# Optimization experiments

Measured on AMD Instinct MI355X. Metric: run time of the kernel, lower is better.

## Reference

```python
import jax, jax.numpy as jnp
import numpy as np

N = 1_000_000
D1 = 16          # n_input_1 (first-layer features, cols 0:16)
D2 = 16          # n_input_2 (second-layer features, cols 16:32)
NC = 64          # n_clusters (first layer)
NCPC = 8         # n_clusters_per_cluster (second layer)


def setup_inputs() -> dict:
    key = jax.random.key(0)
    k1, k2, k3 = jax.random.split(key, 3)
    x = jax.random.normal(k1, (N, D1 + D2), dtype=jnp.float32)
    centers_outer = jax.random.normal(k2, (NC, D1), dtype=jnp.float32)
    centers_inner = jax.random.normal(k3, (NC, NCPC, D2), dtype=jnp.float32)
    return {"x": x, "centers_outer": centers_outer, "centers_inner": centers_inner}


def reference(x, centers_outer, centers_inner):
    # x: [N, D1+D2]; input_1_idx = cols [0:D1], input_2_idx = cols [D1:D1+D2]
    x1 = x[:, :D1]
    x2 = x[:, D1:]

    # First-layer nearest-centroid assignment (squared Euclidean).
    # ||x1 - c||^2 = ||x1||^2 - 2 x1.c + ||c||^2; the ||x1||^2 term is
    # constant over clusters so it does not affect the argmin.
    d1 = jnp.sum(centers_outer ** 2, axis=-1)[None, :] - 2.0 * (x1 @ centers_outer.T)  # [N, NC]
    outer = jnp.argmin(d1, axis=1)  # [N] int

    # Second-layer assignment: each sample only compares against the NCPC
    # sub-centers of its outer cluster (this fuses the original per-cluster
    # torch.where gather/scatter loop into one vectorized pass).
    sub = centers_inner[outer]  # [N, NCPC, D2] gather
    d2 = jnp.sum(sub ** 2, axis=-1) - 2.0 * jnp.einsum("nd,nkd->nk", x2, sub)  # [N, NCPC]
    inner = jnp.argmin(d2, axis=1)  # [N]

    return inner + outer * NCPC  # combined cluster id in [0, NC*NCPC)
```

## Files before the change

kernel.cpp:

```cpp
#include <hip/hip_runtime.h>

constexpr int D = 16;
constexpr int NC = 64;
constexpr int NCPC = 8;
constexpr int OSTRIDE = NCPC * D + 4;
constexpr int NPT = 4;
constexpr int BLOCK = 256;

__global__ __launch_bounds__(BLOCK, 4)
void cluster_kernel(const float* __restrict__ x,
                    const float* __restrict__ co,
                    const float* __restrict__ ci,
                    int* __restrict__ out, int n)
{
    __shared__ __align__(16) float s_ci[NC * OSTRIDE];
    __shared__ __align__(16) float s_onorm[NC];
    __shared__ float s_inorm[NC * 9];

    const int t = threadIdx.x;

    const float4* ci4 = (const float4*)ci;
    #pragma unroll
    for (int i = 0; i < 8; ++i) {
        int idx = t + i * BLOCK;
        int o = idx >> 5;
        int f = idx & 31;
        float4 v = ci4[idx];
        *(float4*)&s_ci[o * OSTRIDE + f * 4] = v;
    }
    for (int i = t; i < NC + NC * NCPC; i += BLOCK) {
        const float* src = (i < NC) ? (co + i * D) : (ci + (i - NC) * D);
        float s = 0.f;
        #pragma unroll
        for (int k = 0; k < D; ++k) s = fmaf(src[k], src[k], s);
        if (i < NC) {
            s_onorm[i] = s;
        } else {
            int ii = i - NC;
            s_inorm[(ii >> 3) * 9 + (ii & 7)] = s;
        }
    }
    __syncthreads();

    const int base = blockIdx.x * (BLOCK * NPT) + t;
    #pragma unroll 1
    for (int it = 0; it < NPT; ++it) {
        int p = base + it * BLOCK;
        if (p < n) {
            const float4* xp = (const float4*)(x + (size_t)p * 32);
            float4 xa = xp[0], xb = xp[1], xc = xp[2], xd = xp[3];
            float4 ya = xp[4], yb = xp[5], yc = xp[6], yd = xp[7];
            float x1[16] = {xa.x,xa.y,xa.z,xa.w, xb.x,xb.y,xb.z,xb.w,
                            xc.x,xc.y,xc.z,xc.w, xd.x,xd.y,xd.z,xd.w};
            float x2[16] = {ya.x,ya.y,ya.z,ya.w, yb.x,yb.y,yb.z,yb.w,
                            yc.x,yc.y,yc.z,yc.w, yd.x,yd.y,yd.z,yd.w};

            float bestd = 3.4e38f;
            int bo = 0;
            #pragma unroll
            for (int jt = 0; jt < NC / 4; ++jt) {
                float4 nn = *(const float4*)&s_onorm[jt * 4];
                #pragma unroll
                for (int jj = 0; jj < 4; ++jj) {
                    int j = jt * 4 + jj;
                    const float* c = co + j * D;
                    float dot = 0.f;
                    #pragma unroll
                    for (int k = 0; k < D; ++k) dot = fmaf(x1[k], c[k], dot);
                    float nrm = (jj == 0) ? nn.x : (jj == 1) ? nn.y : (jj == 2) ? nn.z : nn.w;
                    float d = fmaf(-2.f, dot, nrm);
                    if (d < bestd) { bestd = d; bo = j; }
                }
            }

            const float* cb = s_ci + bo * OSTRIDE;
            const float* nb = s_inorm + bo * 9;
            float bestd2 = 3.4e38f;
            int bk = 0;
            #pragma unroll
            for (int k = 0; k < NCPC; ++k) {
                float4 c0 = *(const float4*)&cb[k * D + 0];
                float4 c1 = *(const float4*)&cb[k * D + 4];
                float4 c2 = *(const float4*)&cb[k * D + 8];
                float4 c3 = *(const float4*)&cb[k * D + 12];
                float dot = 0.f;
                dot = fmaf(x2[0],  c0.x, dot); dot = fmaf(x2[1],  c0.y, dot);
                dot = fmaf(x2[2],  c0.z, dot); dot = fmaf(x2[3],  c0.w, dot);
                dot = fmaf(x2[4],  c1.x, dot); dot = fmaf(x2[5],  c1.y, dot);
                dot = fmaf(x2[6],  c1.z, dot); dot = fmaf(x2[7],  c1.w, dot);
                dot = fmaf(x2[8],  c2.x, dot); dot = fmaf(x2[9],  c2.y, dot);
                dot = fmaf(x2[10], c2.z, dot); dot = fmaf(x2[11], c2.w, dot);
                dot = fmaf(x2[12], c3.x, dot); dot = fmaf(x2[13], c3.y, dot);
                dot = fmaf(x2[14], c3.z, dot); dot = fmaf(x2[15], c3.w, dot);
                float d = fmaf(-2.f, dot, nb[k]);
                if (d < bestd2) { bestd2 = d; bk = k; }
            }

            out[p] = bo * NCPC + bk;
        }
    }
}

extern "C" void kernel_launch(void* const* d_in, const int* in_sizes, int n_in,
                              void* d_out, int out_size, void* d_ws, size_t ws_size,
                              hipStream_t stream) {
    const float* x  = (const float*)d_in[0];
    const float* co = (const float*)d_in[1];
    const float* ci = (const float*)d_in[2];
    int* out = (int*)d_out;
    int n = in_sizes[0] / 32;
    int blocks = (n + BLOCK * NPT - 1) / (BLOCK * NPT);
    cluster_kernel<<<blocks, BLOCK, 0, stream>>>(x, co, ci, out, n);
}
```

Measured before the change: 199.0 us.

## Process four points per thread jointly to reuse outer centroid loads

```diff
diff --git a/kernel.cpp b/kernel.cpp
--- a/kernel.cpp
+++ b/kernel.cpp
@@ -20,84 +20,93 @@
     const int t = threadIdx.x;
 
     const float4* ci4 = (const float4*)ci;
-    #pragma unroll
+#pragma unroll
     for (int i = 0; i < 8; ++i) {
         int idx = t + i * BLOCK;
         int o = idx >> 5;
         int f = idx & 31;
-        float4 v = ci4[idx];
-        *(float4*)&s_ci[o * OSTRIDE + f * 4] = v;
+        *(float4*)&s_ci[o * OSTRIDE + f * 4] = ci4[idx];
     }
     for (int i = t; i < NC + NC * NCPC; i += BLOCK) {
-        const float* src = (i < NC) ? (co + i * D) : (ci + (i - NC) * D);
+        const float* src = (i < NC) ? (co + i * D) : (ci + (size_t)(i - NC) * D);
         float s = 0.f;
-        #pragma unroll
+#pragma unroll
         for (int k = 0; k < D; ++k) s = fmaf(src[k], src[k], s);
-        if (i < NC) {
-            s_onorm[i] = s;
-        } else {
-            int ii = i - NC;
-            s_inorm[(ii >> 3) * 9 + (ii & 7)] = s;
-        }
+        if (i < NC) s_onorm[i] = s;
+        else { int ii = i - NC; s_inorm[(ii >> 3) * 9 + (ii & 7)] = s; }
     }
     __syncthreads();
 
     const int base = blockIdx.x * (BLOCK * NPT) + t;
-    #pragma unroll 1
-    for (int it = 0; it < NPT; ++it) {
-        int p = base + it * BLOCK;
-        if (p < n) {
-            const float4* xp = (const float4*)(x + (size_t)p * 32);
-            float4 xa = xp[0], xb = xp[1], xc = xp[2], xd = xp[3];
-            float4 ya = xp[4], yb = xp[5], yc = xp[6], yd = xp[7];
-            float x1[16] = {xa.x,xa.y,xa.z,xa.w, xb.x,xb.y,xb.z,xb.w,
-                            xc.x,xc.y,xc.z,xc.w, xd.x,xd.y,xd.z,xd.w};
-            float x2[16] = {ya.x,ya.y,ya.z,ya.w, yb.x,yb.y,yb.z,yb.w,
-                            yc.x,yc.y,yc.z,yc.w, yd.x,yd.y,yd.z,yd.w};
 
-            float bestd = 3.4e38f;
-            int bo = 0;
-            #pragma unroll
-            for (int jt = 0; jt < NC / 4; ++jt) {
-                float4 nn = *(const float4*)&s_onorm[jt * 4];
-                #pragma unroll
-                for (int jj = 0; jj < 4; ++jj) {
-                    int j = jt * 4 + jj;
-                    const float* c = co + j * D;
-                    float dot = 0.f;
-                    #pragma unroll
-                    for (int k = 0; k < D; ++k) dot = fmaf(x1[k], c[k], dot);
-                    float nrm = (jj == 0) ? nn.x : (jj == 1) ? nn.y : (jj == 2) ? nn.z : nn.w;
-                    float d = fmaf(-2.f, dot, nrm);
-                    if (d < bestd) { bestd = d; bo = j; }
-                }
-            }
+    int p[NPT];
+    bool valid[NPT];
+#pragma unroll
+    for (int pt = 0; pt < NPT; ++pt) {
+        int pp = base + pt * BLOCK;
+        valid[pt] = pp < n;
+        p[pt] = valid[pt] ? pp : (n - 1);
+    }
 
-            const float* cb = s_ci + bo * OSTRIDE;
-            const float* nb = s_inorm + bo * 9;
-            float bestd2 = 3.4e38f;
-            int bk = 0;
-            #pragma unroll
-            for (int k = 0; k < NCPC; ++k) {
-                float4 c0 = *(const float4*)&cb[k * D + 0];
-                float4 c1 = *(const float4*)&cb[k * D + 4];
-                float4 c2 = *(const float4*)&cb[k * D + 8];
-                float4 c3 = *(const float4*)&cb[k * D + 12];
-                float dot = 0.f;
-                dot = fmaf(x2[0],  c0.x, dot); dot = fmaf(x2[1],  c0.y, dot);
-                dot = fmaf(x2[2],  c0.z, dot); dot = fmaf(x2[3],  c0.w, dot);
-                dot = fmaf(x2[4],  c1.x, dot); dot = fmaf(x2[5],  c1.y, dot);
-                dot = fmaf(x2[6],  c1.z, dot); dot = fmaf(x2[7],  c1.w, dot);
-                dot = fmaf(x2[8],  c2.x, dot); dot = fmaf(x2[9],  c2.y, dot);
-                dot = fmaf(x2[10], c2.z, dot); dot = fmaf(x2[11], c2.w, dot);
-                dot = fmaf(x2[12], c3.x, dot); dot = fmaf(x2[13], c3.y, dot);
-                dot = fmaf(x2[14], c3.z, dot); dot = fmaf(x2[15], c3.w, dot);
-                float d = fmaf(-2.f, dot, nb[k]);
-                if (d < bestd2) { bestd2 = d; bk = k; }
-            }
+    float x1[NPT][D];
+#pragma unroll
+    for (int pt = 0; pt < NPT; ++pt) {
+        const float4* xp = (const float4*)(x + (size_t)p[pt] * 32);
+        float4 a = xp[0], b = xp[1], c = xp[2], d = xp[3];
+        x1[pt][0]=a.x;  x1[pt][1]=a.y;  x1[pt][2]=a.z;  x1[pt][3]=a.w;
+        x1[pt][4]=b.x;  x1[pt][5]=b.y;  x1[pt][6]=b.z;  x1[pt][7]=b.w;
+        x1[pt][8]=c.x;  x1[pt][9]=c.y;  x1[pt][10]=c.z; x1[pt][11]=c.w;
+        x1[pt][12]=d.x; x1[pt][13]=d.y; x1[pt][14]=d.z; x1[pt][15]=d.w;
+    }
 
-            out[p] = bo * NCPC + bk;
+    float bestd[NPT]; int bo[NPT];
+#pragma unroll
+    for (int pt = 0; pt < NPT; ++pt) { bestd[pt] = 3.4e38f; bo[pt] = 0; }
+
+#pragma unroll 2
+    for (int j = 0; j < NC; ++j) {
+        float cj[D];
+#pragma unroll
+        for (int k = 0; k < D; ++k) cj[k] = co[j * D + k];
+        float nrm = s_onorm[j];
+#pragma unroll
+        for (int pt = 0; pt < NPT; ++pt) {
+            float dot = 0.f;
+#pragma unroll
+            for (int k = 0; k < D; ++k) dot = fmaf(x1[pt][k], cj[k], dot);
+            float dd = fmaf(-2.f, dot, nrm);
+            if (dd < bestd[pt]) { bestd[pt] = dd; bo[pt] = j; }
         }
+    }
+
+#pragma unroll
+    for (int pt = 0; pt < NPT; ++pt) {
+        const float4* xp = (const float4*)(x + (size_t)p[pt] * 32);
+        float4 a = xp[4], b = xp[5], c = xp[6], d = xp[7];
+        float x2[D] = {a.x,a.y,a.z,a.w, b.x,b.y,b.z,b.w,
+                       c.x,c.y,c.z,c.w, d.x,d.y,d.z,d.w};
+        const float* cb = s_ci + bo[pt] * OSTRIDE;
+        const float* nb = s_inorm + bo[pt] * 9;
+        float bd = 3.4e38f; int bk = 0;
+#pragma unroll
+        for (int k = 0; k < NCPC; ++k) {
+            float4 c0 = *(const float4*)&cb[k * D + 0];
+            float4 c1 = *(const float4*)&cb[k * D + 4];
+            float4 c2 = *(const float4*)&cb[k * D + 8];
+            float4 c3 = *(const float4*)&cb[k * D + 12];
+            float dot = 0.f;
+            dot = fmaf(x2[0],  c0.x, dot); dot = fmaf(x2[1],  c0.y, dot);
+            dot = fmaf(x2[2],  c0.z, dot); dot = fmaf(x2[3],  c0.w, dot);
+            dot = fmaf(x2[4],  c1.x, dot); dot = fmaf(x2[5],  c1.y, dot);
+            dot = fmaf(x2[6],  c1.z, dot); dot = fmaf(x2[7],  c1.w, dot);
+            dot = fmaf(x2[8],  c2.x, dot); dot = fmaf(x2[9],  c2.y, dot);
+            dot = fmaf(x2[10], c2.z, dot); dot = fmaf(x2[11], c2.w, dot);
+            dot = fmaf(x2[12], c3.x, dot); dot = fmaf(x2[13], c3.y, dot);
+            dot = fmaf(x2[14], c3.z, dot); dot = fmaf(x2[15], c3.w, dot);
+            float dd = fmaf(-2.f, dot, nb[k]);
+            if (dd < bd) { bd = dd; bk = k; }
+        }
+        if (valid[pt]) out[p[pt]] = bo[pt] * NCPC + bk;
     }
 }
 
```

Measured after the change: 205.0 us. 3.0% more time.
